# Performance work log

Hardware: AMD Instinct MI355X
Metric: run time of the kernel (lower is better)

The kernel has to match this reference:

```python
import jax, jax.numpy as jnp
import numpy as np

B, N, C, H = 16, 1024, 768, 12
HD = C // H
SCALE = HD ** -0.5


def setup_inputs() -> dict:
    key = jax.random.key(0)
    k1, k2, k3 = jax.random.split(key, 3)
    x = jax.random.normal(k1, (B, N, C), dtype=jnp.float32)
    W_qkv = jax.random.normal(k2, (C, 3 * C), dtype=jnp.float32) * (C ** -0.5)
    W_proj = jax.random.normal(k3, (C, C), dtype=jnp.float32) * (C ** -0.5)
    b_proj = jnp.zeros((C,), dtype=jnp.float32)
    return {"x": x, "W_qkv": W_qkv, "W_proj": W_proj, "b_proj": b_proj}


def reference(x, W_qkv, W_proj, b_proj):
    # qkv projection: [B, N, 3C] -> chunk into q, k, v
    qkv = x @ W_qkv
    q, k, v = jnp.split(qkv, 3, axis=-1)
    # reshape to [B, H, N, HD]
    q = q.reshape(B, N, H, HD).transpose(0, 2, 1, 3)
    k = k.reshape(B, N, H, HD).transpose(0, 2, 1, 3)
    v = v.reshape(B, N, H, HD).transpose(0, 2, 1, 3)
    # manual attention: scores, softmax, weighted sum
    attn = jnp.einsum("bhqd,bhkd->bhqk", q, k) * SCALE
    attn = jax.nn.softmax(attn, axis=-1)
    out = jnp.einsum("bhqk,bhkd->bhqd", attn, v)
    out = out.transpose(0, 2, 1, 3).reshape(B, N, C)
    # output projection
    return out @ W_proj + b_proj
```

## Files before the change

### kernel.cpp

```cpp
#include <hip/hip_runtime.h>

#define B_   16
#define NH   12
#define SEQ  1024
#define CD   768
#define HD_  64
#define MTOT (B_ * SEQ)
#define QSCALE 0.18033688f

typedef __attribute__((ext_vector_type(4)))  float  f32x4;
typedef __attribute__((ext_vector_type(16))) float  f32x16;
typedef __attribute__((ext_vector_type(8)))  __bf16 bf16x8;
typedef __attribute__((ext_vector_type(2)))  unsigned u32x2;

__device__ __forceinline__ unsigned short f2bf(float f) {
  unsigned u = __float_as_uint(f);
  u = (u + 0x7FFFu + ((u >> 16) & 1u)) >> 16;
  return (unsigned short)u;
}

__device__ __forceinline__ void gload16(const void* g, void* l) {
  __builtin_amdgcn_global_load_lds(
      (const __attribute__((address_space(1))) void*)g,
      (__attribute__((address_space(3))) void*)l, 16, 0, 0);
}

__device__ __forceinline__ u32x2 pswap(unsigned x, unsigned y) {
  return __builtin_amdgcn_permlane32_swap(x, y, false, false);
}


__global__ void cvt_x_kernel(const float* __restrict__ in,
                             unsigned short* __restrict__ out, int n4) {
  int i = blockIdx.x * blockDim.x + threadIdx.x;
  if (i >= n4) return;
  float4 f = reinterpret_cast<const float4*>(in)[i];
  uint2 o;
  o.x = (unsigned)f2bf(f.x) | ((unsigned)f2bf(f.y) << 16);
  o.y = (unsigned)f2bf(f.z) | ((unsigned)f2bf(f.w) << 16);
  reinterpret_cast<uint2*>(out)[i] = o;
}

__global__ void transpose_cvt_kernel(const float* __restrict__ W,
                                     unsigned short* __restrict__ Wt,
                                     int K, int N) {
  __shared__ float tile[32][33];
  int j0 = blockIdx.x * 32, k0 = blockIdx.y * 32;
  int tx = threadIdx.x, ty = threadIdx.y;
  #pragma unroll
  for (int i = 0; i < 4; i++)
    tile[ty + 8 * i][tx] = W[(size_t)(k0 + ty + 8 * i) * N + j0 + tx];
  __syncthreads();
  #pragma unroll
  for (int i = 0; i < 4; i++)
    Wt[(size_t)(j0 + ty + 8 * i) * K + k0 + tx] = f2bf(tile[tx][ty + 8 * i]);
}


__device__ __forceinline__ bf16x8 ldsA64(const unsigned short* buf, int row, int g) {
  int byte = (row << 6) + ((g << 4) ^ (((row >> 1) & 3) << 4));
  return *reinterpret_cast<const bf16x8*>((const char*)buf + byte);
}
__device__ __forceinline__ bf16x8 lds128(const unsigned short* buf, int row, int cb) {
  int byte = (row << 7) + (cb ^ ((row & 7) << 4));
  return *reinterpret_cast<const bf16x8*>((const char*)buf + byte);
}


template <int MODE>
__global__ __launch_bounds__(256, 2)
void gemm_bt_kernel(const unsigned short* __restrict__ A,
                    const unsigned short* __restrict__ Bt, const int K,
                    unsigned short* __restrict__ dstQ,
                    unsigned short* __restrict__ dstK,
                    unsigned short* __restrict__ dstV,
                    float* __restrict__ outF,
                    const float* __restrict__ bias) {
  __shared__ unsigned short As[128 * 32];
  __shared__ unsigned short Bs[128 * 32];
  const int tid = threadIdx.x;
  const int lane = tid & 63;
  const int wave = tid >> 6;
  const int wm = (wave >> 1) << 6;
  const int wn = (wave & 1) << 6;
  const int m0 = blockIdx.x << 7;
  const int j0 = blockIdx.y << 7;

  const int sr = tid >> 2;
  const int sc = (tid & 3) << 4;
  const int scs = sc ^ (((sr >> 1) & 3) << 4);

  f32x4 acc[4][4] = {};

  const char* ab  = (const char*)(A  + (size_t)(m0 + sr) * K) + scs;
  const char* ab2 = (const char*)(A  + (size_t)(m0 + sr + 64) * K) + scs;
  const char* bb  = (const char*)(Bt + (size_t)(j0 + sr) * K) + scs;
  const char* bb2 = (const char*)(Bt + (size_t)(j0 + sr + 64) * K) + scs;

  for (int k0 = 0; k0 < K; k0 += 32) {
    __syncthreads();
    gload16(ab  + k0 * 2, (char*)As + tid * 16);
    gload16(ab2 + k0 * 2, (char*)As + 4096 + tid * 16);
    gload16(bb  + k0 * 2, (char*)Bs + tid * 16);
    gload16(bb2 + k0 * 2, (char*)Bs + 4096 + tid * 16);
    __syncthreads();
    bf16x8 af[4], bf[4];
    const int g = lane >> 4;
    #pragma unroll
    for (int fr = 0; fr < 4; fr++) af[fr] = ldsA64(As, wm + fr * 16 + (lane & 15), g);
    #pragma unroll
    for (int fn = 0; fn < 4; fn++) bf[fn] = ldsA64(Bs, wn + fn * 16 + (lane & 15), g);
    #pragma unroll
    for (int fr = 0; fr < 4; fr++)
      #pragma unroll
      for (int fn = 0; fn < 4; fn++)
        acc[fr][fn] = __builtin_amdgcn_mfma_f32_16x16x32_bf16(af[fr], bf[fn],
                                                              acc[fr][fn], 0, 0, 0);
  }

  #pragma unroll
  for (int fr = 0; fr < 4; fr++) {
    #pragma unroll
    for (int fn = 0; fn < 4; fn++) {
      const int jb = j0 + wn + fn * 16;
      const int jl = jb + (lane & 15);
      const int mb = m0 + wm + fr * 16 + ((lane >> 4) << 2);
      if (MODE == 0) {
        const int sec = jb / CD;
        const int h = (jb - sec * CD) >> 6;
        const int d = jl & 63;
        #pragma unroll
        for (int r = 0; r < 4; r++) {
          const int m = mb + r;
          const int b = m >> 10, n = m & 1023;
          const float v = acc[fr][fn][r];
          if (sec == 0)
            dstQ[((size_t)(b * NH + h) * SEQ + n) * HD_ + d] = f2bf(v * QSCALE);
          else if (sec == 1)
            dstK[((size_t)(b * NH + h) * SEQ + n) * HD_ + d] = f2bf(v);
          else
            dstV[((size_t)(b * NH + h) * HD_ + d) * SEQ + n] = f2bf(v);
        }
      } else {
        const float bv = bias[jl];
        #pragma unroll
        for (int r = 0; r < 4; r++) {
          const int m = mb + r;
          outF[(size_t)m * CD + jl] = acc[fr][fn][r] + bv;
        }
      }
    }
  }
}


__global__ __launch_bounds__(256, 4)
void attn_kernel(const unsigned short* __restrict__ Qg,
                 const unsigned short* __restrict__ Kg,
                 const unsigned short* __restrict__ Vg,
                 unsigned short* __restrict__ Og) {
  __shared__ unsigned short ldsbuf[16384];
  __shared__ float sStat[2][4][32];

  unsigned short* const K0 = ldsbuf;
  unsigned short* const V0 = ldsbuf + 4096;
  unsigned short* const K1 = ldsbuf + 8192;
  unsigned short* const V1 = ldsbuf + 12288;
  unsigned short* const Qs = ldsbuf + 8192;

  const int tid = threadIdx.x;
  const int lane = tid & 63;
  const int wave = tid >> 6;
  const int half = lane >> 5;
  const int q_l = lane & 31;
  const int bh = blockIdx.x;
  const int q0 = blockIdx.y * 128;

  const int sr = tid >> 3;
  const int scs = ((tid & 7) << 4) ^ ((sr & 7) << 4);

  const char* kb0 = (const char*)(Kg + (size_t)bh * SEQ * HD_);
  const char* vb0 = (const char*)(Vg + (size_t)bh * HD_ * SEQ);

  {
    const char* qb = (const char*)(Qg + ((size_t)bh * SEQ + q0) * HD_);
    #pragma unroll
    for (int i = 0; i < 4; i++)
      gload16(qb + (sr + 32 * i) * 128 + scs, (char*)Qs + (tid + 256 * i) * 16);
    gload16(kb0 + sr * 128 + scs, (char*)K0 + tid * 16);
    gload16(kb0 + (sr + 32) * 128 + scs, (char*)K0 + 4096 + tid * 16);
    gload16(vb0 + sr * 2048 + scs, (char*)V0 + tid * 16);
    gload16(vb0 + (sr + 32) * 2048 + scs, (char*)V0 + 4096 + tid * 16);
  }
  __syncthreads();

  bf16x8 qf[4];
  #pragma unroll
  for (int c = 0; c < 4; c++)
    qf[c] = lds128(Qs, wave * 32 + q_l, 32 * c + 16 * half);
  __syncthreads();

  f32x16 o0 = {}, o1 = {};
  float mrun = -1e30f, lrun = 0.f;

  for (int t = 0; t < 16; t++) {
    const unsigned short* const Kc = (t & 1) ? K1 : K0;
    const unsigned short* const Vc = (t & 1) ? V1 : V0;
    unsigned short* const Kn = (t & 1) ? K0 : K1;
    unsigned short* const Vn = (t & 1) ? V0 : V1;
    if (t < 15) {
      const int kv1 = (t + 1) * 64;
      gload16(kb0 + (kv1 + sr) * 128 + scs, (char*)Kn + tid * 16);
      gload16(kb0 + (kv1 + sr + 32) * 128 + scs, (char*)Kn + 4096 + tid * 16);
      gload16(vb0 + sr * 2048 + kv1 * 2 + scs, (char*)Vn + tid * 16);
      gload16(vb0 + (sr + 32) * 2048 + kv1 * 2 + scs, (char*)Vn + 4096 + tid * 16);
    }

    f32x16 s0 = {}, s1 = {};
    #pragma unroll
    for (int c = 0; c < 4; c++) {
      bf16x8 kf0 = lds128(Kc, q_l, 32 * c + 16 * half);
      bf16x8 kf1 = lds128(Kc, 32 + q_l, 32 * c + 16 * half);
      s0 = __builtin_amdgcn_mfma_f32_32x32x16_bf16(kf0, qf[c], s0, 0, 0, 0);
      s1 = __builtin_amdgcn_mfma_f32_32x32x16_bf16(kf1, qf[c], s1, 0, 0, 0);
    }

    float vmax = fmaxf(s0[0], s1[0]);
    #pragma unroll
    for (int r = 1; r < 16; r++) vmax = fmaxf(vmax, fmaxf(s0[r], s1[r]));
    {
      u32x2 mx = pswap(__float_as_uint(vmax), __float_as_uint(vmax));
      vmax = fmaxf(__uint_as_float(mx[0]), __uint_as_float(mx[1]));
    }

    if (!__all(vmax <= mrun + 8.0f)) {
      const float mnew = fmaxf(mrun, vmax);
      const float corr = __builtin_amdgcn_exp2f(mrun - mnew);
      mrun = mnew;
      lrun *= corr;
      if (lane < 32) sStat[0][wave][q_l] = corr;
      f32x4 c4[4];
      #pragma unroll
      for (int j = 0; j < 4; j++)
        c4[j] = *reinterpret_cast<const f32x4*>(&sStat[0][wave][4 * half + 8 * j]);
      #pragma unroll
      for (int r = 0; r < 16; r++) {
        const float cc = c4[r >> 2][r & 3];
        o0[r] *= cc;
        o1[r] *= cc;
      }
    }

    float tsum = 0.f;
    #pragma unroll
    for (int r = 0; r < 16; r++) {
      const float p0 = __builtin_amdgcn_exp2f(s0[r] - mrun);
      const float p1 = __builtin_amdgcn_exp2f(s1[r] - mrun);
      s0[r] = p0; s1[r] = p1;
      tsum += p0 + p1;
    }
    {
      u32x2 ts = pswap(__float_as_uint(tsum), __float_as_uint(tsum));
      tsum = __uint_as_float(ts[0]) + __uint_as_float(ts[1]);
    }
    lrun += tsum;

    unsigned pk[2][8];
    #pragma unroll
    for (int w = 0; w < 8; w++) {
      asm("v_cvt_pk_bf16_f32 %0, %1, %2"
          : "=v"(pk[0][w]) : "v"(s0[2 * w]), "v"(s0[2 * w + 1]));
      asm("v_cvt_pk_bf16_f32 %0, %1, %2"
          : "=v"(pk[1][w]) : "v"(s1[2 * w]), "v"(s1[2 * w + 1]));
    }

    #pragma unroll
    for (int c = 0; c < 4; c++) {
      const int st = c >> 1, cc = c & 1;
      u32x2 rA = pswap(pk[st][4 * cc + 0], pk[st][4 * cc + 2]);
      u32x2 rB = pswap(pk[st][4 * cc + 1], pk[st][4 * cc + 3]);
      union { unsigned u[4]; bf16x8 v; } pa;
      pa.u[0] = rA[0]; pa.u[1] = rB[0]; pa.u[2] = rA[1]; pa.u[3] = rB[1];
      bf16x8 vf0 = lds128(Vc, q_l, 32 * c + 16 * half);
      bf16x8 vf1 = lds128(Vc, 32 + q_l, 32 * c + 16 * half);
      o0 = __builtin_amdgcn_mfma_f32_32x32x16_bf16(pa.v, vf0, o0, 0, 0, 0);
      o1 = __builtin_amdgcn_mfma_f32_32x32x16_bf16(pa.v, vf1, o1, 0, 0, 0);
    }
    __syncthreads();
  }

  if (lane < 32) sStat[1][wave][q_l] = lrun;
  f32x4 rl4[4];
  #pragma unroll
  for (int j = 0; j < 4; j++) {
    f32x4 lv = *reinterpret_cast<const f32x4*>(&sStat[1][wave][4 * half + 8 * j]);
    #pragma unroll
    for (int e = 0; e < 4; e++) rl4[j][e] = __builtin_amdgcn_rcpf(lv[e]);
  }
  const int b = bh / NH, head = bh - b * NH;
  #pragma unroll
  for (int r = 0; r < 16; r++) {
    const int qq = q0 + wave * 32 + (r & 3) + 8 * (r >> 2) + 4 * half;
    const float rl = rl4[r >> 2][r & 3];
    const size_t base = ((size_t)b * SEQ + qq) * CD + head * HD_;
    Og[base + q_l]      = f2bf(o0[r] * rl);
    Og[base + 32 + q_l] = f2bf(o1[r] * rl);
  }
}


extern "C" void kernel_launch(void* const* d_in, const int* in_sizes, int n_in,
                              void* d_out, int out_size, void* d_ws, size_t ws_size,
                              hipStream_t stream) {
  const float* x     = (const float*)d_in[0];
  const float* Wqkv  = (const float*)d_in[1];
  const float* Wproj = (const float*)d_in[2];
  const float* bproj = (const float*)d_in[3];

  char* ws = (char*)d_ws;
  unsigned short* xb  = (unsigned short*)(ws + 0);
  unsigned short* wqT = (unsigned short*)(ws + 25165824);
  unsigned short* wpT = (unsigned short*)(ws + 28704768);
  unsigned short* Qw  = (unsigned short*)(ws + 29884416);
  unsigned short* Kw  = (unsigned short*)(ws + 55050240);
  unsigned short* Vw  = (unsigned short*)(ws + 80216064);
  unsigned short* ao  = (unsigned short*)(ws + 105381888);
  if (ws_size < 130547712ull) return;

  const int n4 = MTOT * CD / 4;
  cvt_x_kernel<<<n4 / 256, 256, 0, stream>>>(x, xb, n4);
  transpose_cvt_kernel<<<dim3(2304 / 32, 768 / 32), dim3(32, 8), 0, stream>>>(Wqkv, wqT, 768, 2304);
  transpose_cvt_kernel<<<dim3(768 / 32, 768 / 32), dim3(32, 8), 0, stream>>>(Wproj, wpT, 768, 768);

  gemm_bt_kernel<0><<<dim3(128, 18), 256, 0, stream>>>(xb, wqT, 768, Qw, Kw, Vw,
                                                       nullptr, nullptr);
  attn_kernel<<<dim3(B_ * NH, SEQ / 128), 256, 0, stream>>>(Qw, Kw, Vw, ao);
  gemm_bt_kernel<1><<<dim3(128, 6), 256, 0, stream>>>(ao, wpT, 768, nullptr, nullptr,
                                                      nullptr, (float*)d_out, bproj);
}
```

Measured before the change: 222.8 us.

## Replace 128x128 GEMM with double-buffered 256x256 tile, 512-thread GEMM

Both projection GEMMs now use a 512-thread kernel with 256x256 output tiles and 64-wide K steps. Global-to-LDS loads are double-buffered with explicit vmcnt waits so loads of the next K tile overlap MFMA work, and MFMA sections are wrapped in s_setprio. The larger tile raises data reuse per LDS load and cuts barriers per FLOP. The cost is 128KB of LDS per block, which limits occupancy, and far fewer blocks (192 for the output projection), which can leave CUs idle.

New measurement: 226.8 us. About the same (+1.8%).

```diff
diff --git a/kernel.cpp b/kernel.cpp
--- a/kernel.cpp
+++ b/kernel.cpp
@@ -12,6 +12,12 @@
 typedef __attribute__((ext_vector_type(16))) float  f32x16;
 typedef __attribute__((ext_vector_type(8)))  __bf16 bf16x8;
 typedef __attribute__((ext_vector_type(2)))  unsigned u32x2;
+
+#define WAITV8 asm volatile("s_waitcnt vmcnt(8)" ::: "memory")
+#define WAITV0 asm volatile("s_waitcnt vmcnt(0)" ::: "memory")
+#define LGKM0  asm volatile("s_waitcnt lgkmcnt(0)" ::: "memory")
+#define BAR    __builtin_amdgcn_s_barrier()
+#define SB0    __builtin_amdgcn_sched_barrier(0)
 
 __device__ __forceinline__ unsigned short f2bf(float f) {
   unsigned u = __float_as_uint(f);
@@ -57,10 +63,6 @@
 }
 
 
-__device__ __forceinline__ bf16x8 ldsA64(const unsigned short* buf, int row, int g) {
-  int byte = (row << 6) + ((g << 4) ^ (((row >> 1) & 3) << 4));
-  return *reinterpret_cast<const bf16x8*>((const char*)buf + byte);
-}
 __device__ __forceinline__ bf16x8 lds128(const unsigned short* buf, int row, int cb) {
   int byte = (row << 7) + (cb ^ ((row & 7) << 4));
   return *reinterpret_cast<const bf16x8*>((const char*)buf + byte);
@@ -68,63 +70,105 @@
 
 
 template <int MODE>
-__global__ __launch_bounds__(256, 2)
-void gemm_bt_kernel(const unsigned short* __restrict__ A,
-                    const unsigned short* __restrict__ Bt, const int K,
+__global__ __launch_bounds__(512, 2)
+void gemm256_kernel(const unsigned short* __restrict__ A,
+                    const unsigned short* __restrict__ Bt,
                     unsigned short* __restrict__ dstQ,
                     unsigned short* __restrict__ dstK,
                     unsigned short* __restrict__ dstV,
                     float* __restrict__ outF,
                     const float* __restrict__ bias) {
-  __shared__ unsigned short As[128 * 32];
-  __shared__ unsigned short Bs[128 * 32];
+  constexpr int K = 768;
+  __shared__ unsigned short lds[65536];
+  unsigned short* const A0 = lds;
+  unsigned short* const Bb0 = lds + 16384;
+  unsigned short* const A1 = lds + 32768;
+  unsigned short* const Bb1 = lds + 49152;
+
   const int tid = threadIdx.x;
   const int lane = tid & 63;
   const int wave = tid >> 6;
-  const int wm = (wave >> 1) << 6;
-  const int wn = (wave & 1) << 6;
-  const int m0 = blockIdx.x << 7;
-  const int j0 = blockIdx.y << 7;
-
-  const int sr = tid >> 2;
-  const int sc = (tid & 3) << 4;
-  const int scs = sc ^ (((sr >> 1) & 3) << 4);
-
-  f32x4 acc[4][4] = {};
-
-  const char* ab  = (const char*)(A  + (size_t)(m0 + sr) * K) + scs;
-  const char* ab2 = (const char*)(A  + (size_t)(m0 + sr + 64) * K) + scs;
-  const char* bb  = (const char*)(Bt + (size_t)(j0 + sr) * K) + scs;
-  const char* bb2 = (const char*)(Bt + (size_t)(j0 + sr + 64) * K) + scs;
-
-  for (int k0 = 0; k0 < K; k0 += 32) {
-    __syncthreads();
-    gload16(ab  + k0 * 2, (char*)As + tid * 16);
-    gload16(ab2 + k0 * 2, (char*)As + 4096 + tid * 16);
-    gload16(bb  + k0 * 2, (char*)Bs + tid * 16);
-    gload16(bb2 + k0 * 2, (char*)Bs + 4096 + tid * 16);
-    __syncthreads();
-    bf16x8 af[4], bf[4];
-    const int g = lane >> 4;
-    #pragma unroll
-    for (int fr = 0; fr < 4; fr++) af[fr] = ldsA64(As, wm + fr * 16 + (lane & 15), g);
-    #pragma unroll
-    for (int fn = 0; fn < 4; fn++) bf[fn] = ldsA64(Bs, wn + fn * 16 + (lane & 15), g);
-    #pragma unroll
-    for (int fr = 0; fr < 4; fr++)
+  const int wm = wave >> 2;
+  const int wn = wave & 3;
+  const int m0 = blockIdx.x << 8;
+  const int j0 = blockIdx.y << 8;
+
+  const int srow = tid >> 3;
+  const int scol = (tid & 7) << 4;
+  const int ssw = scol ^ ((srow & 7) << 4);
+
+  const char* const aS = (const char*)A  + (size_t)(m0 + srow) * (K * 2) + ssw;
+  const char* const bS = (const char*)Bt + (size_t)(j0 + srow) * (K * 2) + ssw;
+
+  f32x4 acc[8][4] = {};
+
+  auto stageT = [&](int kt, unsigned short* Ad, unsigned short* Bd) {
+    const char* as = aS + kt * 128;
+    const char* bs = bS + kt * 128;
+    char* ad = (char*)Ad + srow * 128 + scol;
+    char* bd = (char*)Bd + srow * 128 + scol;
+    #pragma unroll
+    for (int p = 0; p < 4; p++) gload16(as + p * 98304, ad + p * 8192);
+    #pragma unroll
+    for (int p = 0; p < 4; p++) gload16(bs + p * 98304, bd + p * 8192);
+  };
+
+  auto computeT = [&](const unsigned short* Ax, const unsigned short* Bx) {
+    const int fcb = (lane >> 4) << 4;
+    const int rl = lane & 15;
+    bf16x8 bfr[2][4];
+    #pragma unroll
+    for (int ks = 0; ks < 2; ks++)
       #pragma unroll
       for (int fn = 0; fn < 4; fn++)
-        acc[fr][fn] = __builtin_amdgcn_mfma_f32_16x16x32_bf16(af[fr], bf[fn],
-                                                              acc[fr][fn], 0, 0, 0);
-  }
-
-  #pragma unroll
-  for (int fr = 0; fr < 4; fr++) {
+        bfr[ks][fn] = lds128(Bx, wn * 64 + fn * 16 + rl, ks * 64 + fcb);
+    #pragma unroll
+    for (int ks = 0; ks < 2; ks++)
+      #pragma unroll
+      for (int mq = 0; mq < 2; mq++) {
+        bf16x8 af[4];
+        #pragma unroll
+        for (int f = 0; f < 4; f++)
+          af[f] = lds128(Ax, wm * 128 + (mq * 4 + f) * 16 + rl, ks * 64 + fcb);
+        __builtin_amdgcn_s_setprio(1);
+        #pragma unroll
+        for (int f = 0; f < 4; f++)
+          #pragma unroll
+          for (int fn = 0; fn < 4; fn++)
+            acc[mq * 4 + f][fn] = __builtin_amdgcn_mfma_f32_16x16x32_bf16(
+                af[f], bfr[ks][fn], acc[mq * 4 + f][fn], 0, 0, 0);
+        __builtin_amdgcn_s_setprio(0);
+      }
+  };
+
+  stageT(0, A0, Bb0);
+  stageT(1, A1, Bb1);
+
+  #pragma unroll 1
+  for (int t = 0; t < 10; t += 2) {
+    WAITV8; BAR; SB0;
+    computeT(A0, Bb0);
+    SB0; LGKM0; BAR;
+    stageT(t + 2, A0, Bb0);
+
+    WAITV8; BAR; SB0;
+    computeT(A1, Bb1);
+    SB0; LGKM0; BAR;
+    stageT(t + 3, A1, Bb1);
+  }
+  WAITV8; BAR; SB0;
+  computeT(A0, Bb0);
+  SB0;
+  WAITV0; BAR; SB0;
+  computeT(A1, Bb1);
+
+  #pragma unroll
+  for (int fr = 0; fr < 8; fr++) {
     #pragma unroll
     for (int fn = 0; fn < 4; fn++) {
-      const int jb = j0 + wn + fn * 16;
+      const int jb = j0 + wn * 64 + fn * 16;
       const int jl = jb + (lane & 15);
-      const int mb = m0 + wm + fr * 16 + ((lane >> 4) << 2);
+      const int mb = m0 + wm * 128 + fr * 16 + ((lane >> 4) << 2);
       if (MODE == 0) {
         const int sec = jb / CD;
         const int h = (jb - sec * CD) >> 6;
@@ -332,9 +376,9 @@
   transpose_cvt_kernel<<<dim3(2304 / 32, 768 / 32), dim3(32, 8), 0, stream>>>(Wqkv, wqT, 768, 2304);
   transpose_cvt_kernel<<<dim3(768 / 32, 768 / 32), dim3(32, 8), 0, stream>>>(Wproj, wpT, 768, 768);
 
-  gemm_bt_kernel<0><<<dim3(128, 18), 256, 0, stream>>>(xb, wqT, 768, Qw, Kw, Vw,
-                                                       nullptr, nullptr);
+  gemm256_kernel<0><<<dim3(64, 9), 512, 0, stream>>>(xb, wqT, Qw, Kw, Vw,
+                                                     nullptr, nullptr);
   attn_kernel<<<dim3(B_ * NH, SEQ / 128), 256, 0, stream>>>(Qw, Kw, Vw, ao);
-  gemm_bt_kernel<1><<<dim3(128, 6), 256, 0, stream>>>(ao, wpT, 768, nullptr, nullptr,
-                                                      nullptr, (float*)d_out, bproj);
-}
+  gemm256_kernel<1><<<dim3(64, 3), 512, 0, stream>>>(ao, wpT, nullptr, nullptr,
+                                                     nullptr, (float*)d_out, bproj);
+}
```

## Triple-buffer GEMM K-loop and stage QKV epilogue through LDS with coalesced stores

Applied to the files above, without the earlier changes.

The GEMM now fixes K at 768 and uses three LDS buffers, so global-to-LDS loads run up to three tiles ahead, with explicit vmcnt waits and barriers replacing the double __syncthreads per step. The QKV epilogue writes the tile into LDS and then emits 16-byte coalesced stores, Q/K into a row-major [M, 2304] buffer and V into a blocked transposed layout. Previously each bf16 element was scattered individually to per-head Q, K and V buffers. Attention reads Q and K from the row-major buffer with a 4608-byte stride and reads the tiled V layout. The risks are higher LDS use (48KB) and occupancy 3, plus manual waitcnt correctness.

New measurement: 197.6 us. 1.13x faster.

```diff
diff --git a/kernel.cpp b/kernel.cpp
--- a/kernel.cpp
+++ b/kernel.cpp
@@ -12,6 +12,13 @@
 typedef __attribute__((ext_vector_type(16))) float  f32x16;
 typedef __attribute__((ext_vector_type(8)))  __bf16 bf16x8;
 typedef __attribute__((ext_vector_type(2)))  unsigned u32x2;
+
+#define WAITV8 asm volatile("s_waitcnt vmcnt(8)" ::: "memory")
+#define WAITV4 asm volatile("s_waitcnt vmcnt(4)" ::: "memory")
+#define WAITV0 asm volatile("s_waitcnt vmcnt(0)" ::: "memory")
+#define LGKM0  asm volatile("s_waitcnt lgkmcnt(0)" ::: "memory")
+#define BAR    __builtin_amdgcn_s_barrier()
+#define SB0    __builtin_amdgcn_sched_barrier(0)
 
 __device__ __forceinline__ unsigned short f2bf(float f) {
   unsigned u = __float_as_uint(f);
@@ -68,16 +75,22 @@
 
 
 template <int MODE>
-__global__ __launch_bounds__(256, 2)
-void gemm_bt_kernel(const unsigned short* __restrict__ A,
-                    const unsigned short* __restrict__ Bt, const int K,
-                    unsigned short* __restrict__ dstQ,
-                    unsigned short* __restrict__ dstK,
-                    unsigned short* __restrict__ dstV,
+__global__ __launch_bounds__(256, 3)
+void gemm128_kernel(const unsigned short* __restrict__ A,
+                    const unsigned short* __restrict__ Bt,
+                    unsigned short* __restrict__ qkvOut,
+                    unsigned short* __restrict__ vtOut,
                     float* __restrict__ outF,
                     const float* __restrict__ bias) {
-  __shared__ unsigned short As[128 * 32];
-  __shared__ unsigned short Bs[128 * 32];
+  constexpr int K = 768;
+  __shared__ unsigned short sbuf[24576];
+  unsigned short* const A0 = sbuf;
+  unsigned short* const Bb0 = sbuf + 4096;
+  unsigned short* const A1 = sbuf + 8192;
+  unsigned short* const Bb1 = sbuf + 12288;
+  unsigned short* const A2 = sbuf + 16384;
+  unsigned short* const Bb2 = sbuf + 20480;
+
   const int tid = threadIdx.x;
   const int lane = tid & 63;
   const int wave = tid >> 6;
@@ -92,18 +105,20 @@
 
   f32x4 acc[4][4] = {};
 
-  const char* ab  = (const char*)(A  + (size_t)(m0 + sr) * K) + scs;
-  const char* ab2 = (const char*)(A  + (size_t)(m0 + sr + 64) * K) + scs;
-  const char* bb  = (const char*)(Bt + (size_t)(j0 + sr) * K) + scs;
-  const char* bb2 = (const char*)(Bt + (size_t)(j0 + sr + 64) * K) + scs;
-
-  for (int k0 = 0; k0 < K; k0 += 32) {
-    __syncthreads();
-    gload16(ab  + k0 * 2, (char*)As + tid * 16);
-    gload16(ab2 + k0 * 2, (char*)As + 4096 + tid * 16);
-    gload16(bb  + k0 * 2, (char*)Bs + tid * 16);
-    gload16(bb2 + k0 * 2, (char*)Bs + 4096 + tid * 16);
-    __syncthreads();
+  const char* const ab  = (const char*)(A  + (size_t)(m0 + sr) * K) + scs;
+  const char* const ab2 = (const char*)(A  + (size_t)(m0 + sr + 64) * K) + scs;
+  const char* const bb  = (const char*)(Bt + (size_t)(j0 + sr) * K) + scs;
+  const char* const bb2 = (const char*)(Bt + (size_t)(j0 + sr + 64) * K) + scs;
+
+  auto stageT = [&](int kt, unsigned short* Ad, unsigned short* Bd) {
+    const int kb = kt * 64;
+    gload16(ab  + kb, (char*)Ad + tid * 16);
+    gload16(ab2 + kb, (char*)Ad + 4096 + tid * 16);
+    gload16(bb  + kb, (char*)Bd + tid * 16);
+    gload16(bb2 + kb, (char*)Bd + 4096 + tid * 16);
+  };
+
+  auto computeT = [&](const unsigned short* As, const unsigned short* Bs) {
     bf16x8 af[4], bf[4];
     const int g = lane >> 4;
     #pragma unroll
@@ -116,38 +131,91 @@
       for (int fn = 0; fn < 4; fn++)
         acc[fr][fn] = __builtin_amdgcn_mfma_f32_16x16x32_bf16(af[fr], bf[fn],
                                                               acc[fr][fn], 0, 0, 0);
-  }
-
-  #pragma unroll
-  for (int fr = 0; fr < 4; fr++) {
-    #pragma unroll
-    for (int fn = 0; fn < 4; fn++) {
-      const int jb = j0 + wn + fn * 16;
-      const int jl = jb + (lane & 15);
-      const int mb = m0 + wm + fr * 16 + ((lane >> 4) << 2);
-      if (MODE == 0) {
-        const int sec = jb / CD;
-        const int h = (jb - sec * CD) >> 6;
-        const int d = jl & 63;
+  };
+
+  stageT(0, A0, Bb0);
+  stageT(1, A1, Bb1);
+  stageT(2, A2, Bb2);
+
+  #pragma unroll 1
+  for (int t = 0; t < 21; t += 3) {
+    WAITV8; BAR; SB0;
+    computeT(A0, Bb0);
+    SB0; LGKM0; BAR;
+    stageT(t + 3, A0, Bb0);
+
+    WAITV8; BAR; SB0;
+    computeT(A1, Bb1);
+    SB0; LGKM0; BAR;
+    stageT(t + 4, A1, Bb1);
+
+    WAITV8; BAR; SB0;
+    computeT(A2, Bb2);
+    SB0; LGKM0; BAR;
+    stageT(t + 5, A2, Bb2);
+  }
+  WAITV8; BAR; SB0;
+  computeT(A0, Bb0);
+  WAITV4; BAR; SB0;
+  computeT(A1, Bb1);
+  WAITV0; BAR; SB0;
+  computeT(A2, Bb2);
+
+  const int g4 = (lane >> 4) << 2;
+
+  if (MODE == 0) {
+    LGKM0; BAR;
+    const bool secV = (j0 >= 1536);
+    const float scale = (j0 < 768) ? QSCALE : 1.0f;
+    char* const ct = (char*)sbuf;
+    #pragma unroll
+    for (int fr = 0; fr < 4; fr++) {
+      #pragma unroll
+      for (int fn = 0; fn < 4; fn++) {
+        const int j_l = wn + fn * 16 + (lane & 15);
         #pragma unroll
         for (int r = 0; r < 4; r++) {
-          const int m = mb + r;
-          const int b = m >> 10, n = m & 1023;
-          const float v = acc[fr][fn][r];
-          if (sec == 0)
-            dstQ[((size_t)(b * NH + h) * SEQ + n) * HD_ + d] = f2bf(v * QSCALE);
-          else if (sec == 1)
-            dstK[((size_t)(b * NH + h) * SEQ + n) * HD_ + d] = f2bf(v);
-          else
-            dstV[((size_t)(b * NH + h) * HD_ + d) * SEQ + n] = f2bf(v);
+          const int m_l = wm + fr * 16 + g4 + r;
+          const unsigned short v = f2bf(acc[fr][fn][r] * scale);
+          const int addr = secV ? (j_l * 288 + m_l * 2) : (m_l * 288 + j_l * 2);
+          *reinterpret_cast<unsigned short*>(ct + addr) = v;
         }
-      } else {
+      }
+    }
+    LGKM0; BAR;
+    const int c = tid & 15, r0 = tid >> 4;
+    if (!secV) {
+      char* const gb = (char*)qkvOut + (size_t)m0 * 4608 + j0 * 2 + c * 16;
+      #pragma unroll
+      for (int k = 0; k < 8; k++) {
+        const int row = r0 + 16 * k;
+        const uint4 d = *reinterpret_cast<const uint4*>(ct + row * 288 + c * 16);
+        *reinterpret_cast<uint4*>(gb + (size_t)row * 4608) = d;
+      }
+    } else {
+      const int b = m0 >> 10, nblk = (m0 & 1023) >> 7;
+      const int h0 = (j0 - 1536) >> 6;
+      char* const vb = (char*)vtOut +
+          ((size_t)(b * NH + h0) * 65536 + (size_t)nblk * 8192) * 2 + c * 16;
+      #pragma unroll
+      for (int k = 0; k < 8; k++) {
+        const int row = r0 + 16 * k;
+        const uint4 d = *reinterpret_cast<const uint4*>(ct + row * 288 + c * 16);
+        const size_t off = ((size_t)(row >> 6) * 65536 + (size_t)(row & 63) * 128) * 2;
+        *reinterpret_cast<uint4*>(vb + off) = d;
+      }
+    }
+  } else {
+    #pragma unroll
+    for (int fr = 0; fr < 4; fr++) {
+      #pragma unroll
+      for (int fn = 0; fn < 4; fn++) {
+        const int jl = j0 + wn + fn * 16 + (lane & 15);
+        const int mb = m0 + wm + fr * 16 + g4;
         const float bv = bias[jl];
         #pragma unroll
-        for (int r = 0; r < 4; r++) {
-          const int m = mb + r;
-          outF[(size_t)m * CD + jl] = acc[fr][fn][r] + bv;
-        }
+        for (int r = 0; r < 4; r++)
+          outF[(size_t)(mb + r) * CD + jl] = acc[fr][fn][r] + bv;
       }
     }
   }
@@ -155,9 +223,8 @@
 
 
 __global__ __launch_bounds__(256, 4)
-void attn_kernel(const unsigned short* __restrict__ Qg,
-                 const unsigned short* __restrict__ Kg,
-                 const unsigned short* __restrict__ Vg,
+void attn_kernel(const unsigned short* __restrict__ qkvB,
+                 const unsigned short* __restrict__ Vt,
                  unsigned short* __restrict__ Og) {
   __shared__ unsigned short ldsbuf[16384];
   __shared__ float sStat[2][4][32];
@@ -175,22 +242,25 @@
   const int q_l = lane & 31;
   const int bh = blockIdx.x;
   const int q0 = blockIdx.y * 128;
+  const int b = bh / NH, head = bh - b * NH;
 
   const int sr = tid >> 3;
   const int scs = ((tid & 7) << 4) ^ ((sr & 7) << 4);
 
-  const char* kb0 = (const char*)(Kg + (size_t)bh * SEQ * HD_);
-  const char* vb0 = (const char*)(Vg + (size_t)bh * HD_ * SEQ);
+  const char* const xb_ = (const char*)qkvB + (size_t)b * 1024 * 4608;
+  const int qoff = head * 128;
+  const int koff = qoff + 1536;
+  const char* const vb0 = (const char*)Vt + (size_t)bh * 131072;
 
   {
-    const char* qb = (const char*)(Qg + ((size_t)bh * SEQ + q0) * HD_);
     #pragma unroll
     for (int i = 0; i < 4; i++)
-      gload16(qb + (sr + 32 * i) * 128 + scs, (char*)Qs + (tid + 256 * i) * 16);
-    gload16(kb0 + sr * 128 + scs, (char*)K0 + tid * 16);
-    gload16(kb0 + (sr + 32) * 128 + scs, (char*)K0 + 4096 + tid * 16);
-    gload16(vb0 + sr * 2048 + scs, (char*)V0 + tid * 16);
-    gload16(vb0 + (sr + 32) * 2048 + scs, (char*)V0 + 4096 + tid * 16);
+      gload16(xb_ + (size_t)(q0 + sr + 32 * i) * 4608 + qoff + scs,
+              (char*)Qs + (tid + 256 * i) * 16);
+    gload16(xb_ + (size_t)sr * 4608 + koff + scs, (char*)K0 + tid * 16);
+    gload16(xb_ + (size_t)(sr + 32) * 4608 + koff + scs, (char*)K0 + 4096 + tid * 16);
+    gload16(vb0 + sr * 256 + scs, (char*)V0 + tid * 16);
+    gload16(vb0 + (sr + 32) * 256 + scs, (char*)V0 + 4096 + tid * 16);
   }
   __syncthreads();
 
@@ -210,10 +280,12 @@
     unsigned short* const Vn = (t & 1) ? V0 : V1;
     if (t < 15) {
       const int kv1 = (t + 1) * 64;
-      gload16(kb0 + (kv1 + sr) * 128 + scs, (char*)Kn + tid * 16);
-      gload16(kb0 + (kv1 + sr + 32) * 128 + scs, (char*)Kn + 4096 + tid * 16);
-      gload16(vb0 + sr * 2048 + kv1 * 2 + scs, (char*)Vn + tid * 16);
-      gload16(vb0 + (sr + 32) * 2048 + kv1 * 2 + scs, (char*)Vn + 4096 + tid * 16);
+      const char* const vtile = vb0 + (kv1 >> 7) * 16384 + ((kv1 >> 6) & 1) * 128;
+      gload16(xb_ + (size_t)(kv1 + sr) * 4608 + koff + scs, (char*)Kn + tid * 16);
+      gload16(xb_ + (size_t)(kv1 + sr + 32) * 4608 + koff + scs,
+              (char*)Kn + 4096 + tid * 16);
+      gload16(vtile + sr * 256 + scs, (char*)Vn + tid * 16);
+      gload16(vtile + (sr + 32) * 256 + scs, (char*)Vn + 4096 + tid * 16);
     }
 
     f32x16 s0 = {}, s1 = {};
@@ -297,7 +369,6 @@
     #pragma unroll
     for (int e = 0; e < 4; e++) rl4[j][e] = __builtin_amdgcn_rcpf(lv[e]);
   }
-  const int b = bh / NH, head = bh - b * NH;
   #pragma unroll
   for (int r = 0; r < 16; r++) {
     const int qq = q0 + wave * 32 + (r & 3) + 8 * (r >> 2) + 4 * half;
@@ -318,13 +389,12 @@
   const float* bproj = (const float*)d_in[3];
 
   char* ws = (char*)d_ws;
-  unsigned short* xb  = (unsigned short*)(ws + 0);
-  unsigned short* wqT = (unsigned short*)(ws + 25165824);
-  unsigned short* wpT = (unsigned short*)(ws + 28704768);
-  unsigned short* Qw  = (unsigned short*)(ws + 29884416);
-  unsigned short* Kw  = (unsigned short*)(ws + 55050240);
-  unsigned short* Vw  = (unsigned short*)(ws + 80216064);
-  unsigned short* ao  = (unsigned short*)(ws + 105381888);
+  unsigned short* qkvB = (unsigned short*)(ws + 0);
+  unsigned short* Vt   = (unsigned short*)(ws + 75497472);
+  unsigned short* xb   = (unsigned short*)(ws + 100663296);
+  unsigned short* ao   = (unsigned short*)(ws + 100663296);
+  unsigned short* wqT  = (unsigned short*)(ws + 125829120);
+  unsigned short* wpT  = (unsigned short*)(ws + 129368064);
   if (ws_size < 130547712ull) return;
 
   const int n4 = MTOT * CD / 4;
@@ -332,9 +402,9 @@
   transpose_cvt_kernel<<<dim3(2304 / 32, 768 / 32), dim3(32, 8), 0, stream>>>(Wqkv, wqT, 768, 2304);
   transpose_cvt_kernel<<<dim3(768 / 32, 768 / 32), dim3(32, 8), 0, stream>>>(Wproj, wpT, 768, 768);
 
-  gemm_bt_kernel<0><<<dim3(128, 18), 256, 0, stream>>>(xb, wqT, 768, Qw, Kw, Vw,
+  gemm128_kernel<0><<<dim3(128, 18), 256, 0, stream>>>(xb, wqT, qkvB, Vt,
                                                        nullptr, nullptr);
-  attn_kernel<<<dim3(B_ * NH, SEQ / 128), 256, 0, stream>>>(Qw, Kw, Vw, ao);
-  gemm_bt_kernel<1><<<dim3(128, 6), 256, 0, stream>>>(ao, wpT, 768, nullptr, nullptr,
-                                                      nullptr, (float*)d_out, bproj);
-}
+  attn_kernel<<<dim3(B_ * NH, SEQ / 128), 256, 0, stream>>>(qkvB, Vt, ao);
+  gemm128_kernel<1><<<dim3(128, 6), 256, 0, stream>>>(ao, wpT, nullptr, nullptr,
+                                                      (float*)d_out, bproj);
+}
```
